# Kernel tuning notes

Hardware: AMD Instinct MI355X
Metric: run time of the kernel (lower is better)

The kernel has to match this reference:

```python
import jax, jax.numpy as jnp
import numpy as np
import math

FOV, NEAR, FAR = 60.0, 0.1, 100.0
W_RES, H_RES = 128, 128
N_GAUSS = 1024


def _normalize(v):
    return v / (jnp.linalg.norm(v) + 1e-8)


def _view_matrix(pos, look_at, up):
    # Same construction as Camera._compute_view_matrix
    f = _normalize(look_at - pos)
    r = _normalize(jnp.cross(f, up))
    u = _normalize(jnp.cross(r, f))
    return jnp.stack([
        jnp.concatenate([r, -jnp.dot(r, pos)[None]]),
        jnp.concatenate([u, -jnp.dot(u, pos)[None]]),
        jnp.concatenate([-f, jnp.dot(f, pos)[None]]),
        jnp.array([0.0, 0.0, 0.0, 1.0], dtype=pos.dtype),
    ])


def _proj_matrix():
    # Same construction as Camera._compute_projection_matrix
    aspect = W_RES / H_RES
    foc = 1.0 / math.tan(math.radians(FOV) / 2.0)
    P = np.zeros((4, 4), np.float32)
    P[0, 0] = foc / aspect
    P[1, 1] = foc
    P[2, 2] = (FAR + NEAR) / (NEAR - FAR)
    P[2, 3] = 2.0 * FAR * NEAR / (NEAR - FAR)
    P[3, 2] = -1.0
    return jnp.asarray(P)


def _quat_to_rot(q):
    # q: [N,4] (w,x,y,z) -> [N,3,3]
    q = q / (jnp.linalg.norm(q, axis=-1, keepdims=True) + 1e-8)
    w, x, y, z = q[:, 0], q[:, 1], q[:, 2], q[:, 3]
    return jnp.stack([
        jnp.stack([1 - 2 * (y * y + z * z), 2 * (x * y - w * z), 2 * (x * z + w * y)], -1),
        jnp.stack([2 * (x * y + w * z), 1 - 2 * (x * x + z * z), 2 * (y * z - w * x)], -1),
        jnp.stack([2 * (x * z - w * y), 2 * (y * z + w * x), 1 - 2 * (x * x + y * y)], -1),
    ], axis=1)


def _splat(means, log_scales, quats, opacity_logits, colors, cam_position, look_at, up):
    V = _view_matrix(cam_position, look_at, up)
    P = _proj_matrix()

    # 3D covariance: R S S^T R^T
    R = _quat_to_rot(quats)                       # [N,3,3]
    S = jnp.exp(log_scales)                       # [N,3]
    M = R * S[:, None, :]
    cov3d = jnp.einsum('nij,nkj->nik', M, M)      # [N,3,3]

    # Project means to view / clip / pixel space
    mh = jnp.concatenate([means, jnp.ones((means.shape[0], 1), means.dtype)], -1)
    pv = mh @ V.T                                 # [N,4] view space
    tx, ty, tz = pv[:, 0], pv[:, 1], pv[:, 2]     # tz < 0 in front of camera
    depth = -tz
    clip = pv @ P.T
    cw = jnp.where(jnp.abs(clip[:, 3]) < 1e-6, 1e-6, clip[:, 3])
    ndc = clip[:, :2] / cw[:, None]
    px = (ndc[:, 0] + 1.0) * 0.5 * W_RES          # pixel x center
    py = (ndc[:, 1] + 1.0) * 0.5 * H_RES          # pixel y center

    # EWA Jacobian -> 2D covariance
    foc = 1.0 / math.tan(math.radians(FOV) / 2.0)
    fx = foc / (W_RES / H_RES) * (W_RES / 2.0)
    fy = foc * (H_RES / 2.0)
    zsafe = jnp.where(jnp.abs(tz) < 1e-6, 1e-6, tz)
    zero = jnp.zeros_like(zsafe)
    J = jnp.stack([
        jnp.stack([fx / zsafe, zero, -fx * tx / (zsafe * zsafe)], -1),
        jnp.stack([zero, fy / zsafe, -fy * ty / (zsafe * zsafe)], -1),
    ], axis=1)                                    # [N,2,3]
    T = jnp.einsum('nij,jk->nik', J, V[:3, :3])   # [N,2,3]
    cov2d = jnp.einsum('nij,njk,nlk->nil', T, cov3d, T)  # [N,2,2]
    a = cov2d[:, 0, 0] + 0.3
    b = cov2d[:, 0, 1]
    c = cov2d[:, 1, 1] + 0.3
    det = jnp.maximum(a * c - b * b, 1e-6)
    ia, ib, ic = c / det, -b / det, a / det       # inverse 2x2

    # Per-pixel Gaussian weights: [N,H,W]
    u = jnp.arange(W_RES, dtype=means.dtype) + 0.5
    v = jnp.arange(H_RES, dtype=means.dtype) + 0.5
    dx = px[:, None, None] - u[None, None, :]
    dy = py[:, None, None] - v[None, :, None]
    power = -0.5 * (ia[:, None, None] * dx * dx
                    + 2.0 * ib[:, None, None] * dx * dy
                    + ic[:, None, None] * dy * dy)
    opac = jax.nn.sigmoid(opacity_logits)
    w = opac[:, None, None] * jnp.exp(jnp.minimum(power, 0.0))
    valid = (depth > NEAR) & (depth < FAR)
    w = jnp.where(valid[:, None, None], w, 0.0)
    w = jnp.clip(w, 0.0, 0.99)

    # Depth sort (front-to-back) then alpha composite via exclusive cumsum of log(1-a)
    order = jnp.argsort(depth)
    ws = w[order]                                 # [N,H,W]
    cs = jax.nn.sigmoid(colors)[order]            # [N,3]
    ds = depth[order]
    log_om = jnp.log1p(-ws)
    trans = jnp.exp(jnp.cumsum(log_om, axis=0) - log_om)  # exclusive transmittance
    contrib = trans * ws                          # [N,H,W]
    rgb = jnp.einsum('nhw,nc->chw', contrib, cs)  # [3,H,W]
    depth_img = jnp.sum(contrib * ds[:, None, None], axis=0, keepdims=True)
    alpha_img = jnp.sum(contrib, axis=0, keepdims=True)
    # background_color = [0,0,0] so no background term is added
    return rgb, depth_img, alpha_img


def setup_inputs() -> dict:
    key = jax.random.key(0)
    ks = jax.random.split(key, 6)
    means = jax.random.normal(ks[0], (N_GAUSS, 3), jnp.float32) * 1.5
    log_scales = jax.random.normal(ks[1], (N_GAUSS, 3), jnp.float32) * 0.3 - 2.5
    quats = jax.random.normal(ks[2], (N_GAUSS, 4), jnp.float32)
    opacity_logits = jax.random.normal(ks[3], (N_GAUSS,), jnp.float32)
    colors = jax.random.normal(ks[4], (N_GAUSS, 3), jnp.float32)
    cam_position = jnp.array([0.0, 0.0, 5.0], jnp.float32) + 0.05 * jax.random.normal(ks[5], (3,), jnp.float32)
    look_at = jnp.zeros((3,), jnp.float32)
    up = jnp.array([0.0, 1.0, 0.0], jnp.float32)
    return {"means": means, "log_scales": log_scales, "quats": quats,
            "opacity_logits": opacity_logits, "colors": colors,
            "cam_position": cam_position, "look_at": look_at, "up": up}


def reference(means, log_scales, quats, opacity_logits, colors, cam_position, look_at, up):
    return _splat(means, log_scales, quats, opacity_logits, colors, cam_position, look_at, up)
```

## Files before the change

kernel.cpp:

```cpp
#include <hip/hip_runtime.h>
#include <math.h>

#define NG 1024
#define W_RES 128
#define H_RES 128
#define NPIX (W_RES * H_RES)
#define NBLK 8
#define BT (NG / NBLK)
#define TILES_X 8
#define NTILE 64

__device__ float  s_R2[NG];
__device__ float4 s_g0[NG];
__device__ float4 s_g1[NG];
__device__ float4 s_col[NG];

__global__ __launch_bounds__(128) void prep_kernel(
    const float* __restrict__ means, const float* __restrict__ log_scales,
    const float* __restrict__ quats, const float* __restrict__ opacity_logits,
    const float* __restrict__ colors, const float* __restrict__ cam,
    const float* __restrict__ look, const float* __restrict__ up) {
  __shared__ __align__(16) float sdepth[NG];
  const int tid = threadIdx.x;
  const int me = blockIdx.x * BT + tid;

  const float cpx = cam[0], cpy = cam[1], cpz = cam[2];
  float fx0 = look[0] - cpx, fy0 = look[1] - cpy, fz0 = look[2] - cpz;
  float inv = 1.f / (sqrtf(fx0 * fx0 + fy0 * fy0 + fz0 * fz0) + 1e-8f);
  const float fX = fx0 * inv, fY = fy0 * inv, fZ = fz0 * inv;
  const float ux0 = up[0], uy0 = up[1], uz0 = up[2];
  float rX0 = fY * uz0 - fZ * uy0, rY0 = fZ * ux0 - fX * uz0, rZ0 = fX * uy0 - fY * ux0;
  inv = 1.f / (sqrtf(rX0 * rX0 + rY0 * rY0 + rZ0 * rZ0) + 1e-8f);
  const float rX = rX0 * inv, rY = rY0 * inv, rZ = rZ0 * inv;
  float uX0 = rY * fZ - rZ * fY, uY0 = rZ * fX - rX * fZ, uZ0 = rX * fY - rY * fX;
  inv = 1.f / (sqrtf(uX0 * uX0 + uY0 * uY0 + uZ0 * uZ0) + 1e-8f);
  const float uX = uX0 * inv, uY = uY0 * inv, uZ = uZ0 * inv;
  const float V00 = rX, V01 = rY, V02 = rZ, V03 = -(rX * cpx + rY * cpy + rZ * cpz);
  const float V10 = uX, V11 = uY, V12 = uZ, V13 = -(uX * cpx + uY * cpy + uZ * cpz);
  const float V20 = -fX, V21 = -fY, V22 = -fZ, V23 = (fX * cpx + fY * cpy + fZ * cpz);

  const float foc = 1.7320508075688772f;
  const float fpx = foc * 64.f;
  const float fpy = foc * 64.f;

#pragma unroll
  for (int i = 0; i < NG / BT; ++i) {
    const int g = i * BT + tid;
    const float mx = means[3 * g + 0], my = means[3 * g + 1], mz = means[3 * g + 2];
    sdepth[g] = -(V20 * mx + V21 * my + V22 * mz + V23);
  }
  __syncthreads();

  const float dme = sdepth[me];
  int rank = 0;
  const float4* dep4 = (const float4*)sdepth;
#pragma unroll 4
  for (int k = 0; k < NG / 4; ++k) {
    const float4 d4 = dep4[k];
    const int j = 4 * k;
    rank += (d4.x < dme || (d4.x == dme && (j + 0) < me)) ? 1 : 0;
    rank += (d4.y < dme || (d4.y == dme && (j + 1) < me)) ? 1 : 0;
    rank += (d4.z < dme || (d4.z == dme && (j + 2) < me)) ? 1 : 0;
    rank += (d4.w < dme || (d4.w == dme && (j + 3) < me)) ? 1 : 0;
  }

  float qw = quats[4 * me + 0], qx = quats[4 * me + 1], qy = quats[4 * me + 2], qz = quats[4 * me + 3];
  float qinv = 1.f / (sqrtf(qw * qw + qx * qx + qy * qy + qz * qz) + 1e-8f);
  qw *= qinv; qx *= qinv; qy *= qinv; qz *= qinv;
  const float R00 = 1.f - 2.f * (qy * qy + qz * qz), R01 = 2.f * (qx * qy - qw * qz), R02 = 2.f * (qx * qz + qw * qy);
  const float R10 = 2.f * (qx * qy + qw * qz), R11 = 1.f - 2.f * (qx * qx + qz * qz), R12 = 2.f * (qy * qz - qw * qx);
  const float R20 = 2.f * (qx * qz - qw * qy), R21 = 2.f * (qy * qz + qw * qx), R22 = 1.f - 2.f * (qx * qx + qy * qy);
  const float s0 = __expf(log_scales[3 * me + 0]);
  const float s1 = __expf(log_scales[3 * me + 1]);
  const float s2 = __expf(log_scales[3 * me + 2]);
  const float M00 = R00 * s0, M01 = R01 * s1, M02 = R02 * s2;
  const float M10 = R10 * s0, M11 = R11 * s1, M12 = R12 * s2;
  const float M20 = R20 * s0, M21 = R21 * s1, M22 = R22 * s2;
  const float c00 = M00 * M00 + M01 * M01 + M02 * M02;
  const float c01 = M00 * M10 + M01 * M11 + M02 * M12;
  const float c02 = M00 * M20 + M01 * M21 + M02 * M22;
  const float c11 = M10 * M10 + M11 * M11 + M12 * M12;
  const float c12 = M10 * M20 + M11 * M21 + M12 * M22;
  const float c22 = M20 * M20 + M21 * M21 + M22 * M22;
  const float mx = means[3 * me + 0], my = means[3 * me + 1], mz = means[3 * me + 2];
  const float tx = V00 * mx + V01 * my + V02 * mz + V03;
  const float ty = V10 * mx + V11 * my + V12 * mz + V13;
  const float tz = V20 * mx + V21 * my + V22 * mz + V23;
  const float depth = -tz;
  const float cw = (fabsf(depth) < 1e-6f) ? 1e-6f : depth;
  const float pxs = (foc * tx / cw + 1.f) * 0.5f * (float)W_RES;
  const float pys = (foc * ty / cw + 1.f) * 0.5f * (float)H_RES;
  const float zs = (fabsf(tz) < 1e-6f) ? 1e-6f : tz;
  const float J00 = fpx / zs, J02 = -fpx * tx / (zs * zs);
  const float J11 = fpy / zs, J12 = -fpy * ty / (zs * zs);
  const float T00 = J00 * V00 + J02 * V20;
  const float T01 = J00 * V01 + J02 * V21;
  const float T02 = J00 * V02 + J02 * V22;
  const float T10 = J11 * V10 + J12 * V20;
  const float T11 = J11 * V11 + J12 * V21;
  const float T12 = J11 * V12 + J12 * V22;
  const float t00 = T00 * c00 + T01 * c01 + T02 * c02;
  const float t01 = T00 * c01 + T01 * c11 + T02 * c12;
  const float t02 = T00 * c02 + T01 * c12 + T02 * c22;
  const float t10 = T10 * c00 + T11 * c01 + T12 * c02;
  const float t11 = T10 * c01 + T11 * c11 + T12 * c12;
  const float t12 = T10 * c02 + T11 * c12 + T12 * c22;
  const float a  = t00 * T00 + t01 * T01 + t02 * T02 + 0.3f;
  const float bb = t00 * T10 + t01 * T11 + t02 * T12;
  const float c  = t10 * T10 + t11 * T11 + t12 * T12 + 0.3f;
  const float det = fmaxf(a * c - bb * bb, 1e-6f);
  const float ia = c / det, ib = -bb / det, ic = a / det;
  const float op = 1.f / (1.f + __expf(-opacity_logits[me]));
  const bool valid = (depth > 0.1f) && (depth < 100.f);
  const float lam = 0.5f * (a + c) + sqrtf(0.25f * (a - c) * (a - c) + bb * bb);
  float R2v = 2.f * lam * logf(op * 1e7f);
  if (!valid) R2v = -1.f;
  const float logop = logf(op);
  const float cr = 1.f / (1.f + __expf(-colors[3 * me + 0]));
  const float cg = 1.f / (1.f + __expf(-colors[3 * me + 1]));
  const float cb = 1.f / (1.f + __expf(-colors[3 * me + 2]));

  s_R2[rank]  = R2v;
  s_g0[rank]  = make_float4(pxs, pys, -0.5f * ia, -ib);
  s_g1[rank]  = make_float4(-0.5f * ic, logop, depth, 0.f);
  s_col[rank] = make_float4(cr, cg, cb, 0.f);
}

__global__ __launch_bounds__(256) void render_kernel(float* __restrict__ out) {
  __shared__ float4 tg0[NG];
  __shared__ float4 tg1[NG];
  __shared__ float4 tcol[NG];
  __shared__ int scnt[4];
  const int tid = threadIdx.x;
  const int tile = blockIdx.x;
  const int wid = tid >> 6, lane = tid & 63;
  const int ox = (tile & (TILES_X - 1)) * 16;
  const int oy = (tile >> 3) * 16;
  const float x0 = ox + 0.5f, x1 = ox + 15.5f;
  const float y0 = oy + 0.5f, y1 = oy + 15.5f;

  int total = 0;
#pragma unroll
  for (int r = 0; r < 4; ++r) {
    const int g = r * 256 + tid;
    const float4 g0 = s_g0[g];
    const float r2 = s_R2[g];
    const float nx = fminf(fmaxf(g0.x, x0), x1);
    const float ny = fminf(fmaxf(g0.y, y0), y1);
    const float ddx = nx - g0.x, ddy = ny - g0.y;
    const bool surv = (ddx * ddx + ddy * ddy) <= r2;
    const unsigned long long m = __ballot(surv);
    if (lane == 0) scnt[wid] = __popcll(m);
    __syncthreads();
    int base = total;
    for (int w = 0; w < wid; ++w) base += scnt[w];
    total += scnt[0] + scnt[1] + scnt[2] + scnt[3];
    if (surv) {
      const int pos = base + __popcll(m & ((1ull << lane) - 1ull));
      tg0[pos] = g0;
      tg1[pos] = s_g1[g];
      tcol[pos] = s_col[g];
    }
    __syncthreads();
  }

  const int lx = tid & 15, ly = tid >> 4;
  const float u = (float)(ox + lx) + 0.5f;
  const float v = (float)(oy + ly) + 0.5f;
  float T = 1.f, ar = 0.f, ag = 0.f, ab = 0.f, ad = 0.f, aa = 0.f;
  for (int s = 0; s < total; ++s) {
    const float4 g0 = tg0[s];
    const float4 g1 = tg1[s];
    const float4 cc = tcol[s];
    const float dx = g0.x - u, dy = g0.y - v;
    float pw = dx * (g0.z * dx + g0.w * dy) + g1.x * dy * dy;
    pw = fminf(pw, 0.f) + g1.y;
    const float w = fminf(__expf(pw), 0.99f);
    const float ctr = T * w;
    ar += ctr * cc.x; ag += ctr * cc.y; ab += ctr * cc.z;
    ad += ctr * g1.z; aa += ctr;
    T *= (1.f - w);
  }
  const int p = (oy + ly) * W_RES + (ox + lx);
  out[0 * NPIX + p] = ar;
  out[1 * NPIX + p] = ag;
  out[2 * NPIX + p] = ab;
  out[3 * NPIX + p] = ad;
  out[4 * NPIX + p] = aa;
}

extern "C" void kernel_launch(void* const* d_in, const int* in_sizes, int n_in,
                              void* d_out, int out_size, void* d_ws, size_t ws_size,
                              hipStream_t stream) {
  const float* means = (const float*)d_in[0];
  const float* log_scales = (const float*)d_in[1];
  const float* quats = (const float*)d_in[2];
  const float* opacity_logits = (const float*)d_in[3];
  const float* colors = (const float*)d_in[4];
  const float* cam = (const float*)d_in[5];
  const float* look = (const float*)d_in[6];
  const float* up = (const float*)d_in[7];
  float* out = (float*)d_out;

  prep_kernel<<<NBLK, BT, 0, stream>>>(means, log_scales, quats, opacity_logits,
                                       colors, cam, look, up);
  render_kernel<<<NTILE, 256, 0, stream>>>(out);
}
```

Measured before the change: 111.0 us.

## Fuse preprocessing into per-tile render kernel with local depth sort

Merges the per-Gaussian preprocessing kernel into the tile render kernel. Each tile block recomputes projection and covariance for all 1024 Gaussians, culls them, and ranks only the survivors by depth in shared memory. This removes one kernel launch, the global-memory round trip, and the global all-pairs rank, at the cost of redundant preprocessing in all 64 blocks. It also adds an O(survivors²) per-tile sort and an indirect sperm lookup in the blend loop.

Result: faster. 104.5 us (-5.9%).

```diff
diff --git a/kernel.cpp b/kernel.cpp
--- a/kernel.cpp
+++ b/kernel.cpp
@@ -5,24 +5,29 @@
 #define W_RES 128
 #define H_RES 128
 #define NPIX (W_RES * H_RES)
-#define NBLK 8
-#define BT (NG / NBLK)
+#define NTILE 64
 #define TILES_X 8
-#define NTILE 64
 
-__device__ float  s_R2[NG];
-__device__ float4 s_g0[NG];
-__device__ float4 s_g1[NG];
-__device__ float4 s_col[NG];
-
-__global__ __launch_bounds__(128) void prep_kernel(
+__global__ __launch_bounds__(256) void splat_kernel(
     const float* __restrict__ means, const float* __restrict__ log_scales,
     const float* __restrict__ quats, const float* __restrict__ opacity_logits,
     const float* __restrict__ colors, const float* __restrict__ cam,
-    const float* __restrict__ look, const float* __restrict__ up) {
-  __shared__ __align__(16) float sdepth[NG];
+    const float* __restrict__ look, const float* __restrict__ up,
+    float* __restrict__ out) {
+  __shared__ float4 tg0[NG];
+  __shared__ float4 tg1[NG];
+  __shared__ float4 tcol[NG];
+  __shared__ float  skey[NG];
+  __shared__ int    sidx[NG];
+  __shared__ int    sperm[NG];
+  __shared__ int    scnt[4];
   const int tid = threadIdx.x;
-  const int me = blockIdx.x * BT + tid;
+  const int wid = tid >> 6, lane = tid & 63;
+  const int tile = blockIdx.x;
+  const int ox = (tile & (TILES_X - 1)) * 16;
+  const int oy = (tile >> 3) * 16;
+  const float x0 = ox + 0.5f, x1 = ox + 15.5f;
+  const float y0 = oy + 0.5f, y1 = oy + 15.5f;
 
   const float cpx = cam[0], cpy = cam[1], cpz = cam[2];
   float fx0 = look[0] - cpx, fy0 = look[1] - cpy, fz0 = look[2] - cpz;
@@ -38,117 +43,70 @@
   const float V00 = rX, V01 = rY, V02 = rZ, V03 = -(rX * cpx + rY * cpy + rZ * cpz);
   const float V10 = uX, V11 = uY, V12 = uZ, V13 = -(uX * cpx + uY * cpy + uZ * cpz);
   const float V20 = -fX, V21 = -fY, V22 = -fZ, V23 = (fX * cpx + fY * cpy + fZ * cpz);
-
   const float foc = 1.7320508075688772f;
-  const float fpx = foc * 64.f;
-  const float fpy = foc * 64.f;
-
-#pragma unroll
-  for (int i = 0; i < NG / BT; ++i) {
-    const int g = i * BT + tid;
-    const float mx = means[3 * g + 0], my = means[3 * g + 1], mz = means[3 * g + 2];
-    sdepth[g] = -(V20 * mx + V21 * my + V22 * mz + V23);
-  }
-  __syncthreads();
-
-  const float dme = sdepth[me];
-  int rank = 0;
-  const float4* dep4 = (const float4*)sdepth;
-#pragma unroll 4
-  for (int k = 0; k < NG / 4; ++k) {
-    const float4 d4 = dep4[k];
-    const int j = 4 * k;
-    rank += (d4.x < dme || (d4.x == dme && (j + 0) < me)) ? 1 : 0;
-    rank += (d4.y < dme || (d4.y == dme && (j + 1) < me)) ? 1 : 0;
-    rank += (d4.z < dme || (d4.z == dme && (j + 2) < me)) ? 1 : 0;
-    rank += (d4.w < dme || (d4.w == dme && (j + 3) < me)) ? 1 : 0;
-  }
-
-  float qw = quats[4 * me + 0], qx = quats[4 * me + 1], qy = quats[4 * me + 2], qz = quats[4 * me + 3];
-  float qinv = 1.f / (sqrtf(qw * qw + qx * qx + qy * qy + qz * qz) + 1e-8f);
-  qw *= qinv; qx *= qinv; qy *= qinv; qz *= qinv;
-  const float R00 = 1.f - 2.f * (qy * qy + qz * qz), R01 = 2.f * (qx * qy - qw * qz), R02 = 2.f * (qx * qz + qw * qy);
-  const float R10 = 2.f * (qx * qy + qw * qz), R11 = 1.f - 2.f * (qx * qx + qz * qz), R12 = 2.f * (qy * qz - qw * qx);
-  const float R20 = 2.f * (qx * qz - qw * qy), R21 = 2.f * (qy * qz + qw * qx), R22 = 1.f - 2.f * (qx * qx + qy * qy);
-  const float s0 = __expf(log_scales[3 * me + 0]);
-  const float s1 = __expf(log_scales[3 * me + 1]);
-  const float s2 = __expf(log_scales[3 * me + 2]);
-  const float M00 = R00 * s0, M01 = R01 * s1, M02 = R02 * s2;
-  const float M10 = R10 * s0, M11 = R11 * s1, M12 = R12 * s2;
-  const float M20 = R20 * s0, M21 = R21 * s1, M22 = R22 * s2;
-  const float c00 = M00 * M00 + M01 * M01 + M02 * M02;
-  const float c01 = M00 * M10 + M01 * M11 + M02 * M12;
-  const float c02 = M00 * M20 + M01 * M21 + M02 * M22;
-  const float c11 = M10 * M10 + M11 * M11 + M12 * M12;
-  const float c12 = M10 * M20 + M11 * M21 + M12 * M22;
-  const float c22 = M20 * M20 + M21 * M21 + M22 * M22;
-  const float mx = means[3 * me + 0], my = means[3 * me + 1], mz = means[3 * me + 2];
-  const float tx = V00 * mx + V01 * my + V02 * mz + V03;
-  const float ty = V10 * mx + V11 * my + V12 * mz + V13;
-  const float tz = V20 * mx + V21 * my + V22 * mz + V23;
-  const float depth = -tz;
-  const float cw = (fabsf(depth) < 1e-6f) ? 1e-6f : depth;
-  const float pxs = (foc * tx / cw + 1.f) * 0.5f * (float)W_RES;
-  const float pys = (foc * ty / cw + 1.f) * 0.5f * (float)H_RES;
-  const float zs = (fabsf(tz) < 1e-6f) ? 1e-6f : tz;
-  const float J00 = fpx / zs, J02 = -fpx * tx / (zs * zs);
-  const float J11 = fpy / zs, J12 = -fpy * ty / (zs * zs);
-  const float T00 = J00 * V00 + J02 * V20;
-  const float T01 = J00 * V01 + J02 * V21;
-  const float T02 = J00 * V02 + J02 * V22;
-  const float T10 = J11 * V10 + J12 * V20;
-  const float T11 = J11 * V11 + J12 * V21;
-  const float T12 = J11 * V12 + J12 * V22;
-  const float t00 = T00 * c00 + T01 * c01 + T02 * c02;
-  const float t01 = T00 * c01 + T01 * c11 + T02 * c12;
-  const float t02 = T00 * c02 + T01 * c12 + T02 * c22;
-  const float t10 = T10 * c00 + T11 * c01 + T12 * c02;
-  const float t11 = T10 * c01 + T11 * c11 + T12 * c12;
-  const float t12 = T10 * c02 + T11 * c12 + T12 * c22;
-  const float a  = t00 * T00 + t01 * T01 + t02 * T02 + 0.3f;
-  const float bb = t00 * T10 + t01 * T11 + t02 * T12;
-  const float c  = t10 * T10 + t11 * T11 + t12 * T12 + 0.3f;
-  const float det = fmaxf(a * c - bb * bb, 1e-6f);
-  const float ia = c / det, ib = -bb / det, ic = a / det;
-  const float op = 1.f / (1.f + __expf(-opacity_logits[me]));
-  const bool valid = (depth > 0.1f) && (depth < 100.f);
-  const float lam = 0.5f * (a + c) + sqrtf(0.25f * (a - c) * (a - c) + bb * bb);
-  float R2v = 2.f * lam * logf(op * 1e7f);
-  if (!valid) R2v = -1.f;
-  const float logop = logf(op);
-  const float cr = 1.f / (1.f + __expf(-colors[3 * me + 0]));
-  const float cg = 1.f / (1.f + __expf(-colors[3 * me + 1]));
-  const float cb = 1.f / (1.f + __expf(-colors[3 * me + 2]));
-
-  s_R2[rank]  = R2v;
-  s_g0[rank]  = make_float4(pxs, pys, -0.5f * ia, -ib);
-  s_g1[rank]  = make_float4(-0.5f * ic, logop, depth, 0.f);
-  s_col[rank] = make_float4(cr, cg, cb, 0.f);
-}
-
-__global__ __launch_bounds__(256) void render_kernel(float* __restrict__ out) {
-  __shared__ float4 tg0[NG];
-  __shared__ float4 tg1[NG];
-  __shared__ float4 tcol[NG];
-  __shared__ int scnt[4];
-  const int tid = threadIdx.x;
-  const int tile = blockIdx.x;
-  const int wid = tid >> 6, lane = tid & 63;
-  const int ox = (tile & (TILES_X - 1)) * 16;
-  const int oy = (tile >> 3) * 16;
-  const float x0 = ox + 0.5f, x1 = ox + 15.5f;
-  const float y0 = oy + 0.5f, y1 = oy + 15.5f;
+  const float fpx = foc * 64.f, fpy = foc * 64.f;
 
   int total = 0;
-#pragma unroll
   for (int r = 0; r < 4; ++r) {
     const int g = r * 256 + tid;
-    const float4 g0 = s_g0[g];
-    const float r2 = s_R2[g];
-    const float nx = fminf(fmaxf(g0.x, x0), x1);
-    const float ny = fminf(fmaxf(g0.y, y0), y1);
-    const float ddx = nx - g0.x, ddy = ny - g0.y;
-    const bool surv = (ddx * ddx + ddy * ddy) <= r2;
+    const float mx = means[3 * g + 0], my = means[3 * g + 1], mz = means[3 * g + 2];
+    const float tx = V00 * mx + V01 * my + V02 * mz + V03;
+    const float ty = V10 * mx + V11 * my + V12 * mz + V13;
+    const float tz = V20 * mx + V21 * my + V22 * mz + V23;
+    const float depth = -tz;
+    const float cw = (fabsf(depth) < 1e-6f) ? 1e-6f : depth;
+    const float pxs = (foc * tx / cw + 1.f) * 0.5f * (float)W_RES;
+    const float pys = (foc * ty / cw + 1.f) * 0.5f * (float)H_RES;
+
+    float qw = quats[4 * g + 0], qx = quats[4 * g + 1], qy = quats[4 * g + 2], qz = quats[4 * g + 3];
+    const float qinv = 1.f / (sqrtf(qw * qw + qx * qx + qy * qy + qz * qz) + 1e-8f);
+    qw *= qinv; qx *= qinv; qy *= qinv; qz *= qinv;
+    const float R00 = 1.f - 2.f * (qy * qy + qz * qz), R01 = 2.f * (qx * qy - qw * qz), R02 = 2.f * (qx * qz + qw * qy);
+    const float R10 = 2.f * (qx * qy + qw * qz), R11 = 1.f - 2.f * (qx * qx + qz * qz), R12 = 2.f * (qy * qz - qw * qx);
+    const float R20 = 2.f * (qx * qz - qw * qy), R21 = 2.f * (qy * qz + qw * qx), R22 = 1.f - 2.f * (qx * qx + qy * qy);
+    const float s0 = __expf(log_scales[3 * g + 0]);
+    const float s1 = __expf(log_scales[3 * g + 1]);
+    const float s2 = __expf(log_scales[3 * g + 2]);
+    const float M00 = R00 * s0, M01 = R01 * s1, M02 = R02 * s2;
+    const float M10 = R10 * s0, M11 = R11 * s1, M12 = R12 * s2;
+    const float M20 = R20 * s0, M21 = R21 * s1, M22 = R22 * s2;
+    const float c00 = M00 * M00 + M01 * M01 + M02 * M02;
+    const float c01 = M00 * M10 + M01 * M11 + M02 * M12;
+    const float c02 = M00 * M20 + M01 * M21 + M02 * M22;
+    const float c11 = M10 * M10 + M11 * M11 + M12 * M12;
+    const float c12 = M10 * M20 + M11 * M21 + M12 * M22;
+    const float c22 = M20 * M20 + M21 * M21 + M22 * M22;
+    const float zs = (fabsf(tz) < 1e-6f) ? 1e-6f : tz;
+    const float J00 = fpx / zs, J02 = -fpx * tx / (zs * zs);
+    const float J11 = fpy / zs, J12 = -fpy * ty / (zs * zs);
+    const float T00 = J00 * V00 + J02 * V20;
+    const float T01 = J00 * V01 + J02 * V21;
+    const float T02 = J00 * V02 + J02 * V22;
+    const float T10 = J11 * V10 + J12 * V20;
+    const float T11 = J11 * V11 + J12 * V21;
+    const float T12 = J11 * V12 + J12 * V22;
+    const float t00 = T00 * c00 + T01 * c01 + T02 * c02;
+    const float t01 = T00 * c01 + T01 * c11 + T02 * c12;
+    const float t02 = T00 * c02 + T01 * c12 + T02 * c22;
+    const float t10 = T10 * c00 + T11 * c01 + T12 * c02;
+    const float t11 = T10 * c01 + T11 * c11 + T12 * c12;
+    const float t12 = T10 * c02 + T11 * c12 + T12 * c22;
+    const float a  = t00 * T00 + t01 * T01 + t02 * T02 + 0.3f;
+    const float bb = t00 * T10 + t01 * T11 + t02 * T12;
+    const float c  = t10 * T10 + t11 * T11 + t12 * T12 + 0.3f;
+    const float det = fmaxf(a * c - bb * bb, 1e-6f);
+    const float ia = c / det, ib = -bb / det, ic = a / det;
+    const float op = 1.f / (1.f + __expf(-opacity_logits[g]));
+    const bool valid = (depth > 0.1f) && (depth < 100.f);
+    const float lam = 0.5f * (a + c) + sqrtf(0.25f * (a - c) * (a - c) + bb * bb);
+    float R2v = 2.f * lam * logf(op * 1e7f);
+    if (!valid) R2v = -1.f;
+
+    const float nx = fminf(fmaxf(pxs, x0), x1);
+    const float ny = fminf(fmaxf(pys, y0), y1);
+    const float ddx = nx - pxs, ddy = ny - pys;
+    const bool surv = (ddx * ddx + ddy * ddy) <= R2v;
+
     const unsigned long long m = __ballot(surv);
     if (lane == 0) scnt[wid] = __popcll(m);
     __syncthreads();
@@ -157,18 +115,35 @@
     total += scnt[0] + scnt[1] + scnt[2] + scnt[3];
     if (surv) {
       const int pos = base + __popcll(m & ((1ull << lane) - 1ull));
-      tg0[pos] = g0;
-      tg1[pos] = s_g1[g];
-      tcol[pos] = s_col[g];
+      tg0[pos] = make_float4(pxs, pys, -0.5f * ia, -ib);
+      tg1[pos] = make_float4(-0.5f * ic, logf(op), depth, 0.f);
+      tcol[pos] = make_float4(1.f / (1.f + __expf(-colors[3 * g + 0])),
+                              1.f / (1.f + __expf(-colors[3 * g + 1])),
+                              1.f / (1.f + __expf(-colors[3 * g + 2])), 0.f);
+      skey[pos] = depth;
+      sidx[pos] = g;
     }
     __syncthreads();
   }
+
+  for (int s = tid; s < total; s += 256) {
+    const float d = skey[s];
+    const int id = sidx[s];
+    int rank = 0;
+    for (int j = 0; j < total; ++j) {
+      const float dj = skey[j];
+      rank += (dj < d || (dj == d && sidx[j] < id)) ? 1 : 0;
+    }
+    sperm[rank] = s;
+  }
+  __syncthreads();
 
   const int lx = tid & 15, ly = tid >> 4;
   const float u = (float)(ox + lx) + 0.5f;
   const float v = (float)(oy + ly) + 0.5f;
   float T = 1.f, ar = 0.f, ag = 0.f, ab = 0.f, ad = 0.f, aa = 0.f;
-  for (int s = 0; s < total; ++s) {
+  for (int t = 0; t < total; ++t) {
+    const int s = sperm[t];
     const float4 g0 = tg0[s];
     const float4 g1 = tg1[s];
     const float4 cc = tcol[s];
@@ -202,7 +177,6 @@
   const float* up = (const float*)d_in[7];
   float* out = (float*)d_out;
 
-  prep_kernel<<<NBLK, BT, 0, stream>>>(means, log_scales, quats, opacity_logits,
-                                       colors, cam, look, up);
-  render_kernel<<<NTILE, 256, 0, stream>>>(out);
+  splat_kernel<<<NTILE, 256, 0, stream>>>(means, log_scales, quats, opacity_logits,
+                                          colors, cam, look, up, out);
 }
```
